# Kernel optimization log

Measured on AMD Instinct MI355X. Metric: run time of the kernel, lower is better.

Reference implementation:

```python
import jax, jax.numpy as jnp
import numpy as np

B, T, V, H = 32, 2048, 64, 256
HD = H // 2  # per-direction hidden (bidirectional GRU)


def setup_inputs() -> dict:
    key = jax.random.key(0)
    ks = jax.random.split(key, 8)
    s = 0.1
    return {
        "tokens": jax.random.randint(ks[0], (B, T), 0, V, dtype=jnp.int32),
        "lengths": jax.random.randint(ks[1], (B,), 1, T + 1, dtype=jnp.int32),
        "emb": jax.random.normal(ks[2], (V, H), jnp.float32) * s,
        "Wih_f": jax.random.normal(ks[3], (3 * HD, H), jnp.float32) * s,
        "Whh_f": jax.random.normal(ks[4], (3 * HD, HD), jnp.float32) * s,
        "bih_f": jnp.zeros((3 * HD,), jnp.float32),
        "bhh_f": jnp.zeros((3 * HD,), jnp.float32),
        "Wih_b": jax.random.normal(ks[5], (3 * HD, H), jnp.float32) * s,
        "Whh_b": jax.random.normal(ks[6], (3 * HD, HD), jnp.float32) * s,
        "bih_b": jnp.zeros((3 * HD,), jnp.float32),
        "bhh_b": jnp.zeros((3 * HD,), jnp.float32),
    }


def _gru_dir(x, mask, Wih, Whh, bih, bhh):
    # x: [B,T,H] inputs, mask: [B,T] valid positions; torch GRU cell math.
    b, t, _ = x.shape
    hd = Whh.shape[1]
    h0 = jnp.zeros((b, hd), x.dtype)

    def step(h, inp):
        x_t, m_t = inp  # [B,H], [B,1]
        gi = x_t @ Wih.T + bih
        gh = h @ Whh.T + bhh
        gi_r, gi_z, gi_n = jnp.split(gi, 3, axis=-1)
        gh_r, gh_z, gh_n = jnp.split(gh, 3, axis=-1)
        r = jax.nn.sigmoid(gi_r + gh_r)
        z = jax.nn.sigmoid(gi_z + gh_z)
        n = jnp.tanh(gi_n + r * gh_n)
        h_new = (1 - z) * n + z * h
        h = jnp.where(m_t, h_new, h)  # freeze state past sequence end
        return h, h

    _, outs = jax.lax.scan(step, h0, (x.transpose(1, 0, 2), mask.T[:, :, None]))
    return outs.transpose(1, 0, 2)  # [B,T,HD]


def reference(tokens, lengths, emb, Wih_f, Whh_f, bih_f, bhh_f, Wih_b, Whh_b, bih_b, bhh_b):
    lengths = jnp.maximum(lengths, 1)
    x = emb[tokens]  # [B,T,H] embedding lookup
    t_idx = jnp.arange(tokens.shape[1])
    mask = t_idx[None, :] < lengths[:, None]  # [B,T]
    # forward direction
    out_f = _gru_dir(x, mask, Wih_f, Whh_f, bih_f, bhh_f)
    # backward direction: reverse each sequence within its valid region
    ridx = jnp.clip(lengths[:, None] - 1 - t_idx[None, :], 0)  # [B,T]
    x_rev = jnp.take_along_axis(x, ridx[:, :, None], axis=1)
    out_b_rev = _gru_dir(x_rev, mask, Wih_b, Whh_b, bih_b, bhh_b)
    out_b = jnp.take_along_axis(out_b_rev, ridx[:, :, None], axis=1)
    out = jnp.concatenate([out_f, out_b], axis=-1)  # [B,T,H] (torch concat order: fwd, bwd)
    # mean pool over valid timesteps (matches .mean(0) per variable-length sequence)
    denom = lengths[:, None].astype(out.dtype)
    pooled = (out * mask[:, :, None]).sum(axis=1) / denom  # [B,H]
    return pooled
```

## Files before the change

### kernel.cpp

```cpp
#include <hip/hip_runtime.h>

#define BB 32
#define TT 2048
#define VV 64
#define HH 256
#define HD 128
#define G3 384

__device__ __forceinline__ float fsigmoid(float x) {
  return __builtin_amdgcn_rcpf(1.0f + __expf(-x));
}
__device__ __forceinline__ float ftanh(float x) {
  float ax = fabsf(x);
  float t = __expf(-2.0f * ax);
  float r = 1.0f - 2.0f * t * __builtin_amdgcn_rcpf(1.0f + t);
  return copysignf(r, x);
}

__device__ __forceinline__ float quad_reduce_add(float v) {
  int x = __builtin_amdgcn_mov_dpp(__float_as_int(v), 0xB1, 0xF, 0xF, true);
  v += __int_as_float(x);
  x = __builtin_amdgcn_mov_dpp(__float_as_int(v), 0x4E, 0xF, 0xF, true);
  v += __int_as_float(x);
  return v;
}

__global__ __launch_bounds__(G3, 1)
void gi_table_kernel(const float* __restrict__ emb,
                     const float* __restrict__ Wih_f, const float* __restrict__ bih_f,
                     const float* __restrict__ Wih_b, const float* __restrict__ bih_b,
                     float* __restrict__ gi_ws) {
  const int gid = blockIdx.x;
  const int dir = gid >> 6;
  const int v   = gid & 63;
  const int j   = threadIdx.x;
  const float* Wih = dir ? Wih_b : Wih_f;
  const float* bih = dir ? bih_b : bih_f;
  const float4* er = reinterpret_cast<const float4*>(emb + v * HH);
  const float4* wr = reinterpret_cast<const float4*>(Wih + j * HH);
  float acc = bih[j];
  #pragma unroll 8
  for (int k = 0; k < HH / 4; ++k) {
    float4 e = er[k];
    float4 w = wr[k];
    acc = fmaf(e.x, w.x, acc);
    acc = fmaf(e.y, w.y, acc);
    acc = fmaf(e.z, w.z, acc);
    acc = fmaf(e.w, w.w, acc);
  }
  gi_ws[dir * (VV * G3) + v * G3 + j] = acc;
}

__global__ __launch_bounds__(512, 2)
void gru_kernel(const int* __restrict__ tokens, const int* __restrict__ lengths,
                const float* __restrict__ Whh_f, const float* __restrict__ bhh_f,
                const float* __restrict__ Whh_b, const float* __restrict__ bhh_b,
                const float* __restrict__ gi_ws, float* __restrict__ out) {
  __shared__ float giL[VV * G3];
  __shared__ int   tokL[TT];
  __shared__ __align__(16) float hbuf[2][HD];

  const int bid  = blockIdx.x;
  const int b    = bid & 31;
  const int dir  = bid >> 5;
  const int tid  = threadIdx.x;
  const int wave = tid >> 6;
  const int lane = tid & 63;
  const int quad = lane >> 2;
  const int p    = lane & 3;
  const int i    = wave * 16 + quad;

  int len = lengths[b];
  if (len < 1) len = 1;

  const float* gi_src = gi_ws + dir * (VV * G3);
  for (int idx = tid; idx < VV * G3; idx += 512) giL[idx] = gi_src[idx];
  const int* tb = tokens + b * TT;
  for (int s = tid; s < len; s += 512) tokL[s] = tb[dir ? (len - 1 - s) : s];
  if (tid < HD) hbuf[0][tid] = 0.0f;

  const float* Whh = dir ? Whh_b : Whh_f;
  const float* bhh = dir ? bhh_b : bhh_f;
  float4 w4[3][8];
  #pragma unroll
  for (int g = 0; g < 3; ++g) {
    const float4* wr = reinterpret_cast<const float4*>(Whh + (g * HD + i) * HD);
    #pragma unroll
    for (int c = 0; c < 8; ++c) {
      const int k4 = p * 8 + ((c + 2 * p) & 7);
      w4[g][c] = wr[k4];
    }
  }
  const float bhr = bhh[i], bhz = bhh[HD + i], bhn = bhh[2 * HD + i];

  __syncthreads();

  float h = 0.0f, hsum = 0.0f;

  #pragma unroll 2
  for (int s = 0; s < len; ++s) {
    const int cur = s & 1;
    const int tok = tokL[s];
    const float* gi = giL + tok * G3;
    const float gir = gi[i];
    const float giz = gi[HD + i];
    const float gin = gi[2 * HD + i];

    float accr = bhr, accz = bhz, accn = bhn;
    const float4* hb4 = reinterpret_cast<const float4*>(&hbuf[cur][0]);
    #pragma unroll
    for (int c = 0; c < 8; ++c) {
      const float4 hv = hb4[p * 8 + ((c + 2 * p) & 7)];
      accr = fmaf(w4[0][c].x, hv.x, accr);
      accr = fmaf(w4[0][c].y, hv.y, accr);
      accr = fmaf(w4[0][c].z, hv.z, accr);
      accr = fmaf(w4[0][c].w, hv.w, accr);
      accz = fmaf(w4[1][c].x, hv.x, accz);
      accz = fmaf(w4[1][c].y, hv.y, accz);
      accz = fmaf(w4[1][c].z, hv.z, accz);
      accz = fmaf(w4[1][c].w, hv.w, accz);
      accn = fmaf(w4[2][c].x, hv.x, accn);
      accn = fmaf(w4[2][c].y, hv.y, accn);
      accn = fmaf(w4[2][c].z, hv.z, accn);
      accn = fmaf(w4[2][c].w, hv.w, accn);
    }
    accr = quad_reduce_add(accr);
    accz = quad_reduce_add(accz);
    accn = quad_reduce_add(accn);

    const float r = fsigmoid(gir + accr);
    const float z = fsigmoid(giz + accz);
    const float n = ftanh(gin + r * accn);
    h = (1.0f - z) * n + z * h;
    hsum += h;
    if (p == 0) hbuf[cur ^ 1][i] = h;
    __syncthreads();
  }

  if (p == 0) out[b * HH + dir * HD + i] = hsum / (float)len;
}

extern "C" void kernel_launch(void* const* d_in, const int* in_sizes, int n_in,
                              void* d_out, int out_size, void* d_ws, size_t ws_size,
                              hipStream_t stream) {
  const int*   tokens  = (const int*)d_in[0];
  const int*   lengths = (const int*)d_in[1];
  const float* emb     = (const float*)d_in[2];
  const float* Wih_f   = (const float*)d_in[3];
  const float* Whh_f   = (const float*)d_in[4];
  const float* bih_f   = (const float*)d_in[5];
  const float* bhh_f   = (const float*)d_in[6];
  const float* Wih_b   = (const float*)d_in[7];
  const float* Whh_b   = (const float*)d_in[8];
  const float* bih_b   = (const float*)d_in[9];
  const float* bhh_b   = (const float*)d_in[10];
  float* out   = (float*)d_out;
  float* gi_ws = (float*)d_ws;

  gi_table_kernel<<<2 * VV, G3, 0, stream>>>(emb, Wih_f, bih_f, Wih_b, bih_b, gi_ws);
  gru_kernel<<<2 * BB, 512, 0, stream>>>(tokens, lengths, Whh_f, bhh_f, Whh_b, bhh_b,
                                         gi_ws, out);
}
```

Baseline: 970.8 us.

## Use fp16 packed dot products for recurrent matvec and prefetch next-step gate inputs

Stores the recurrent weights in registers as fp16 and the shared hidden-state buffer as fp16, then computes the recurrent matvec with v_dot2 fp16 instructions that accumulate in fp32. This halves the LDS bytes read per step and the number of dot instructions, and frees VGPRs. It also prefetches the next step's token and input-gate values before the barrier to take LDS latency off the serial critical path. Rounding the hidden state to fp16 at every step can build up error over sequences of up to 2048 steps.

```diff
diff --git a/kernel.cpp b/kernel.cpp
--- a/kernel.cpp
+++ b/kernel.cpp
@@ -6,6 +6,9 @@
 #define HH 256
 #define HD 128
 #define G3 384
+
+typedef _Float16 h2 __attribute__((ext_vector_type(2)));
+typedef _Float16 h8 __attribute__((ext_vector_type(8)));
 
 __device__ __forceinline__ float fsigmoid(float x) {
   return __builtin_amdgcn_rcpf(1.0f + __expf(-x));
@@ -23,6 +26,11 @@
   x = __builtin_amdgcn_mov_dpp(__float_as_int(v), 0x4E, 0xF, 0xF, true);
   v += __int_as_float(x);
   return v;
+}
+
+template <int D>
+__device__ __forceinline__ h2 getpair(h8 v) {
+  return __builtin_shufflevector(v, v, 2 * D, 2 * D + 1);
 }
 
 __global__ __launch_bounds__(G3, 1)
@@ -58,7 +66,7 @@
                 const float* __restrict__ gi_ws, float* __restrict__ out) {
   __shared__ float giL[VV * G3];
   __shared__ int   tokL[TT];
-  __shared__ __align__(16) float hbuf[2][HD];
+  __shared__ __align__(16) _Float16 hbufh[2][HD];
 
   const int bid  = blockIdx.x;
   const int b    = bid & 31;
@@ -77,18 +85,21 @@
   for (int idx = tid; idx < VV * G3; idx += 512) giL[idx] = gi_src[idx];
   const int* tb = tokens + b * TT;
   for (int s = tid; s < len; s += 512) tokL[s] = tb[dir ? (len - 1 - s) : s];
-  if (tid < HD) hbuf[0][tid] = 0.0f;
+  if (tid < HD) hbufh[0][tid] = (_Float16)0.0f;
 
   const float* Whh = dir ? Whh_b : Whh_f;
   const float* bhh = dir ? bhh_b : bhh_f;
-  float4 w4[3][8];
+  h8 w8[3][4];
   #pragma unroll
   for (int g = 0; g < 3; ++g) {
-    const float4* wr = reinterpret_cast<const float4*>(Whh + (g * HD + i) * HD);
+    const float* wr = Whh + (g * HD + i) * HD + p * 32;
     #pragma unroll
-    for (int c = 0; c < 8; ++c) {
-      const int k4 = p * 8 + ((c + 2 * p) & 7);
-      w4[g][c] = wr[k4];
+    for (int c = 0; c < 4; ++c) {
+      const int kb = ((c + p) & 3) * 8;
+      h8 w;
+      #pragma unroll
+      for (int d = 0; d < 8; ++d) w[d] = (_Float16)wr[kb + d];
+      w8[g][c] = w;
     }
   }
   const float bhr = bhh[i], bhz = bhh[HD + i], bhn = bhh[2 * HD + i];
@@ -97,33 +108,37 @@
 
   float h = 0.0f, hsum = 0.0f;
 
+  int tok = tokL[0];
+  float gir = giL[tok * G3 + i];
+  float giz = giL[tok * G3 + HD + i];
+  float gin = giL[tok * G3 + 2 * HD + i];
+
+#define DOT8(acc, wv, hv)                                            \
+  acc = __builtin_amdgcn_fdot2(getpair<0>(wv), getpair<0>(hv), acc, false); \
+  acc = __builtin_amdgcn_fdot2(getpair<1>(wv), getpair<1>(hv), acc, false); \
+  acc = __builtin_amdgcn_fdot2(getpair<2>(wv), getpair<2>(hv), acc, false); \
+  acc = __builtin_amdgcn_fdot2(getpair<3>(wv), getpair<3>(hv), acc, false)
+
   #pragma unroll 2
   for (int s = 0; s < len; ++s) {
     const int cur = s & 1;
-    const int tok = tokL[s];
-    const float* gi = giL + tok * G3;
-    const float gir = gi[i];
-    const float giz = gi[HD + i];
-    const float gin = gi[2 * HD + i];
+    const h8* hb8 = reinterpret_cast<const h8*>(&hbufh[cur][0]);
 
     float accr = bhr, accz = bhz, accn = bhn;
-    const float4* hb4 = reinterpret_cast<const float4*>(&hbuf[cur][0]);
     #pragma unroll
-    for (int c = 0; c < 8; ++c) {
-      const float4 hv = hb4[p * 8 + ((c + 2 * p) & 7)];
-      accr = fmaf(w4[0][c].x, hv.x, accr);
-      accr = fmaf(w4[0][c].y, hv.y, accr);
-      accr = fmaf(w4[0][c].z, hv.z, accr);
-      accr = fmaf(w4[0][c].w, hv.w, accr);
-      accz = fmaf(w4[1][c].x, hv.x, accz);
-      accz = fmaf(w4[1][c].y, hv.y, accz);
-      accz = fmaf(w4[1][c].z, hv.z, accz);
-      accz = fmaf(w4[1][c].w, hv.w, accz);
-      accn = fmaf(w4[2][c].x, hv.x, accn);
-      accn = fmaf(w4[2][c].y, hv.y, accn);
-      accn = fmaf(w4[2][c].z, hv.z, accn);
-      accn = fmaf(w4[2][c].w, hv.w, accn);
+    for (int c = 0; c < 4; ++c) {
+      const h8 hv = hb8[p * 4 + ((c + p) & 3)];
+      DOT8(accr, w8[0][c], hv);
+      DOT8(accz, w8[1][c], hv);
+      DOT8(accn, w8[2][c], hv);
     }
+
+    const int sn = (s + 1 < len) ? (s + 1) : 0;
+    const int ntok = tokL[sn];
+    const float ngir = giL[ntok * G3 + i];
+    const float ngiz = giL[ntok * G3 + HD + i];
+    const float ngin = giL[ntok * G3 + 2 * HD + i];
+
     accr = quad_reduce_add(accr);
     accz = quad_reduce_add(accz);
     accn = quad_reduce_add(accn);
@@ -133,9 +148,12 @@
     const float n = ftanh(gin + r * accn);
     h = (1.0f - z) * n + z * h;
     hsum += h;
-    if (p == 0) hbuf[cur ^ 1][i] = h;
+    if (p == 0) hbufh[cur ^ 1][i] = (_Float16)h;
     __syncthreads();
+
+    gir = ngir; giz = ngiz; gin = ngin;
   }
+#undef DOT8
 
   if (p == 0) out[b * HH + dir * HD + i] = hsum / (float)len;
 }
```

Result: faster. 949.7 us (-2.2%).
